# Performance work log

Hardware: AMD Instinct MI355X
Metric: run time of the kernel (lower is better)

Reference implementation:

```python
import jax, jax.numpy as jnp
import numpy as np

N_EMBD = 1024
N_HEAD = 16
HEAD_DIM = N_EMBD // N_HEAD


def setup_inputs() -> dict:
    key = jax.random.key(0)
    kx, kq, kk, kv, ko = jax.random.split(key, 5)
    B, S = 2, 2048
    return {
        "x": jax.random.normal(kx, (B, S, N_EMBD), dtype=jnp.float32),
        "W_q": jax.random.normal(kq, (N_EMBD, N_EMBD), dtype=jnp.float32),
        "W_k": jax.random.normal(kk, (N_EMBD, N_EMBD), dtype=jnp.float32),
        "W_v": jax.random.normal(kv, (N_EMBD, N_EMBD), dtype=jnp.float32),
        "W_o": jax.random.normal(ko, (N_EMBD, N_EMBD), dtype=jnp.float32),
    }


def reference(x, W_q, W_k, W_v, W_o):
    B, S, E = x.shape
    H, D = N_HEAD, HEAD_DIM
    scale = 1.0 / np.sqrt(D).astype(np.float32)
    # QKV projections, split into heads: (B, H, S, D)
    q = (x @ W_q).reshape(B, S, H, D).transpose(0, 2, 1, 3)
    k = (x @ W_k).reshape(B, S, H, D).transpose(0, 2, 1, 3)
    v = (x @ W_v).reshape(B, S, H, D).transpose(0, 2, 1, 3)
    # scaled scores with causal mask
    scores = jnp.einsum("bhqd,bhkd->bhqk", q, k) * scale
    causal = jnp.tril(jnp.ones((S, S), dtype=bool))
    scores = jnp.where(causal, scores, -jnp.inf)
    attn = jax.nn.softmax(scores, axis=-1)
    out = jnp.einsum("bhqk,bhkd->bhqd", attn, v)
    out = out.transpose(0, 2, 1, 3).reshape(B, S, E)
    return out @ W_o
```

## Files before the change

### kernel.cpp

```cpp
#include <hip/hip_runtime.h>
#include <stdint.h>

#define E 1024
#define S 2048
#define NH 16
#define HD 64

typedef _Float16 f16;
typedef _Float16 f16x4 __attribute__((ext_vector_type(4)));
typedef _Float16 f16x8 __attribute__((ext_vector_type(8)));
typedef __fp16 hv4 __attribute__((ext_vector_type(4)));
typedef float f32x4 __attribute__((ext_vector_type(4)));

__device__ __forceinline__ void async16(const void* g, void* l) {
  __builtin_amdgcn_global_load_lds(
      (const __attribute__((address_space(1))) unsigned int*)g,
      (__attribute__((address_space(3))) unsigned int*)l, 16, 0, 0);
}


__global__ __launch_bounds__(256) void cvt_x(const float* __restrict__ x,
                                             f16* __restrict__ xh,
                                             f16* __restrict__ xl) {
  int i = (blockIdx.x * 256 + threadIdx.x) * 4;
  float4 a = *(const float4*)(x + i);
  f16 h0 = (f16)a.x, h1 = (f16)a.y, h2 = (f16)a.z, h3 = (f16)a.w;
  f16x4 hv = {h0, h1, h2, h3};
  f16x4 lv = {(f16)(a.x - (float)h0), (f16)(a.y - (float)h1),
              (f16)(a.z - (float)h2), (f16)(a.w - (float)h3)};
  *(f16x4*)(xh + i) = hv;
  *(f16x4*)(xl + i) = lv;
}

__global__ __launch_bounds__(256) void cvt_w(const float* __restrict__ Wq,
                                             const float* __restrict__ Wk,
                                             const float* __restrict__ Wv,
                                             const float* __restrict__ Wo,
                                             f16* __restrict__ Wh,
                                             f16* __restrict__ Wl) {
  __shared__ float tile[32][33];
  const int z = blockIdx.z;
  const float* W = z == 0 ? Wq : z == 1 ? Wk : z == 2 ? Wv : Wo;
  const int tx = threadIdx.x, ty = threadIdx.y;
  const int x0 = blockIdx.x * 32, y0 = blockIdx.y * 32;
#pragma unroll
  for (int i = 0; i < 4; i++)
    tile[ty + i * 8][tx] = W[(size_t)(y0 + ty + i * 8) * E + x0 + tx];
  __syncthreads();
  f16* outh = Wh + (size_t)z * E * E;
  f16* outl = Wl + (size_t)z * E * E;
#pragma unroll
  for (int i = 0; i < 4; i++) {
    float v = tile[tx][ty + i * 8];
    size_t o = (size_t)(x0 + ty + i * 8) * E + (y0 + tx);
    f16 hi = (f16)v;
    outh[o] = hi;
    if (z < 2) outl[o] = (f16)(v - (float)hi);
  }
}


template <bool SPLIT2>
__device__ __forceinline__ void gemm_mainloop(
    const f16* __restrict__ Ah, const f16* __restrict__ Al,
    const f16* __restrict__ Bh, const f16* __restrict__ Bl, int m0, int n0,
    int K, f16* Ahs, f16* Als, f16* Bhs, f16* Bls, f32x4 acc[4][4]) {
  const int tid = threadIdx.x, lane = tid & 63, wid = tid >> 6;
  const int quad = lane >> 4, c16 = lane & 15;
  const int rA = tid >> 2;
  const int cA = (tid & 3) ^ ((rA >> 1) & 3);
  const size_t gA0 = (size_t)(m0 + rA) * K + cA * 8;
  const size_t gA1 = (size_t)(m0 + 64 + rA) * K + cA * 8;
  const size_t gB0 = (size_t)(n0 + rA) * K + cA * 8;
  const size_t gB1 = (size_t)(n0 + 64 + rA) * K + cA * 8;
  const int l0 = tid * 8, l1 = (256 + tid) * 8;
  int a_off[4], b_off[4];
#pragma unroll
  for (int i = 0; i < 4; i++) {
    int ra = (wid >> 1) * 64 + i * 16 + c16;
    a_off[i] = ra * 32 + ((quad ^ ((ra >> 1) & 3)) << 3);
    int rb = (wid & 1) * 64 + i * 16 + c16;
    b_off[i] = rb * 32 + ((quad ^ ((rb >> 1) & 3)) << 3);
  }
  for (int k0 = 0; k0 < K; k0 += 32) {
    __syncthreads();
    async16(Ah + gA0 + k0, Ahs + l0);
    async16(Ah + gA1 + k0, Ahs + l1);
    async16(Bh + gB0 + k0, Bhs + l0);
    async16(Bh + gB1 + k0, Bhs + l1);
    if constexpr (SPLIT2) {
      async16(Al + gA0 + k0, Als + l0);
      async16(Al + gA1 + k0, Als + l1);
      async16(Bl + gB0 + k0, Bls + l0);
      async16(Bl + gB1 + k0, Bls + l1);
    }
    __syncthreads();
    f16x8 ah[4], bh[4];
#pragma unroll
    for (int i = 0; i < 4; i++) {
      ah[i] = *(const f16x8*)(Ahs + a_off[i]);
      bh[i] = *(const f16x8*)(Bhs + b_off[i]);
    }
    if constexpr (SPLIT2) {
      f16x8 al[4], bl[4];
#pragma unroll
      for (int i = 0; i < 4; i++) {
        al[i] = *(const f16x8*)(Als + a_off[i]);
        bl[i] = *(const f16x8*)(Bls + b_off[i]);
      }
#pragma unroll
      for (int i = 0; i < 4; i++)
#pragma unroll
        for (int j = 0; j < 4; j++) {
          acc[i][j] = __builtin_amdgcn_mfma_f32_16x16x32_f16(ah[i], bh[j], acc[i][j], 0, 0, 0);
          acc[i][j] = __builtin_amdgcn_mfma_f32_16x16x32_f16(ah[i], bl[j], acc[i][j], 0, 0, 0);
          acc[i][j] = __builtin_amdgcn_mfma_f32_16x16x32_f16(al[i], bh[j], acc[i][j], 0, 0, 0);
        }
    } else {
#pragma unroll
      for (int i = 0; i < 4; i++)
#pragma unroll
        for (int j = 0; j < 4; j++)
          acc[i][j] = __builtin_amdgcn_mfma_f32_16x16x32_f16(ah[i], bh[j], acc[i][j], 0, 0, 0);
    }
  }
}

__global__ __launch_bounds__(256) void qkv_gemm(
    const f16* __restrict__ xh, const f16* __restrict__ xl,
    const f16* __restrict__ Wh, const f16* __restrict__ Wl,
    f16* __restrict__ Qh, f16* __restrict__ Ql, f16* __restrict__ Kh,
    f16* __restrict__ Kl, f16* __restrict__ Vt) {
  __shared__ __align__(16) char smem_raw[36864];
  f16* Ahs = (f16*)smem_raw;
  f16* Als = Ahs + 4096;
  f16* Bhs = Ahs + 8192;
  f16* Bls = Ahs + 12288;
  const int z = blockIdx.z;
  const int m0 = blockIdx.y * 128, n0 = blockIdx.x * 128;
  const f16* Bth = Wh + (size_t)z * E * E;
  const f16* Btl = Wl + (size_t)z * E * E;
  f32x4 acc[4][4];
  const f32x4 zero4 = {0.f, 0.f, 0.f, 0.f};
#pragma unroll
  for (int i = 0; i < 4; i++)
#pragma unroll
    for (int j = 0; j < 4; j++) acc[i][j] = zero4;
  if (z < 2)
    gemm_mainloop<true>(xh, xl, Bth, Btl, m0, n0, E, Ahs, Als, Bhs, Bls, acc);
  else
    gemm_mainloop<false>(xh, nullptr, Bth, nullptr, m0, n0, E, Ahs, Als, Bhs, Bls, acc);
  const int tid = threadIdx.x, lane = tid & 63, wid = tid >> 6;
  const int quad = lane >> 4, c16 = lane & 15;
  __syncthreads();
  f16* vbuf = (f16*)smem_raw + (size_t)wid * 4608;
  if (z == 2) {
#pragma unroll
    for (int i = 0; i < 4; i++)
#pragma unroll
      for (int j = 0; j < 4; j++)
#pragma unroll
        for (int r = 0; r < 4; r++) {
          int sl = i * 16 + quad * 4 + r;
          int dl = j * 16 + c16;
          vbuf[dl * 72 + sl] = (f16)acc[i][j][r];
        }
#pragma unroll
    for (int i2 = 0; i2 < 8; i2++) {
      int dl = i2 * 8 + (lane >> 3);
      int ck = lane & 7;
      f16x8 v8 = *(const f16x8*)(vbuf + dl * 72 + ck * 8);
      int dg = n0 + (wid & 1) * 64 + dl;
      int sg = m0 + (wid >> 1) * 64 + ck * 8;
      int b = sg >> 11, s = sg & (S - 1);
      int h = dg >> 6, d = dg & 63;
      *(f16x8*)(Vt + (((size_t)(b * NH + h) * HD + d) << 11) + s) = v8;
    }
  } else {
    const int t0 = m0 + (wid >> 1) * 64;
    const int h = (n0 + (wid & 1) * 64) >> 6;
    const float sc = 0.42466090014400953f;
    f16* dsth = (z == 0) ? Qh : Kh;
    f16* dstl = (z == 0) ? Ql : Kl;
#pragma unroll
    for (int pass = 0; pass < 2; pass++) {
#pragma unroll
      for (int i = 0; i < 4; i++)
#pragma unroll
        for (int j = 0; j < 4; j++)
#pragma unroll
          for (int r = 0; r < 4; r++) {
            float v = acc[i][j][r] * sc;
            f16 hi = (f16)v;
            f16 outv = (pass == 0) ? hi : (f16)(v - (float)hi);
            vbuf[(i * 16 + quad * 4 + r) * 72 + j * 16 + c16] = outv;
          }
      f16* dst = (pass == 0) ? dsth : dstl;
#pragma unroll
      for (int it = 0; it < 8; it++) {
        int row = it * 8 + (lane >> 3);
        int ck = lane & 7;
        f16x8 v8 = *(const f16x8*)(vbuf + row * 72 + ck * 8);
        int tok = t0 + row;
        int b = tok >> 11, s = tok & (S - 1);
        *(f16x8*)(dst + (((size_t)(b * NH + h) * S + s) << 6) + ck * 8) = v8;
      }
    }
  }
}

__global__ __launch_bounds__(256, 3) void flash(
    const f16* __restrict__ Qh, const f16* __restrict__ Ql,
    const f16* __restrict__ Kh, const f16* __restrict__ Kl,
    const f16* __restrict__ Vt, f16* __restrict__ Ao) {
  __shared__ __align__(16) f16 Khs[2][4096], Kls[2][4096], Vs[2][4096];
  const int tid = threadIdx.x, lane = tid & 63, wid = tid >> 6;
  const int quad = lane >> 4, c16 = lane & 15;
  const int flat = blockIdx.y * 32 + blockIdx.x;
  const int xcd = flat & 7, slot = flat >> 3;
  const int bh = xcd * 4 + (slot >> 5);
  const int qtile = 31 - (slot & 31);
  const int q0 = qtile * 64;
  const size_t bhoff = (size_t)bh * S * HD;
  const int qbase = wid * 16;
  f16x8 qf_h[2], qf_l[2];
#pragma unroll
  for (int ks = 0; ks < 2; ks++) {
    int q = q0 + qbase + c16;
    size_t off = bhoff + (size_t)q * HD + ks * 32 + quad * 8;
    qf_h[ks] = *(const f16x8*)(Qh + off);
    qf_l[ks] = *(const f16x8*)(Ql + off);
  }
  const int niter = qtile + 1;
  const int s0 = tid, s1 = 256 + tid;
  const int r0 = s0 >> 3, cc0 = ((s0 & 7) ^ (r0 & 7)) * 8;
  const int r1 = s1 >> 3, cc1 = ((s1 & 7) ^ (r1 & 7)) * 8;
  auto stage = [&](int it, int b) {
    const size_t kb = bhoff + (size_t)(it * 64) * HD;
    async16(Kh + kb + r0 * HD + cc0, &Khs[b][s0 * 8]);
    async16(Kh + kb + r1 * HD + cc1, &Khs[b][s1 * 8]);
    async16(Kl + kb + r0 * HD + cc0, &Kls[b][s0 * 8]);
    async16(Kl + kb + r1 * HD + cc1, &Kls[b][s1 * 8]);
    const size_t vb = bhoff + (size_t)(it * 64);
    async16(Vt + vb + (size_t)r0 * S + cc0, &Vs[b][s0 * 8]);
    async16(Vt + vb + (size_t)r1 * S + cc1, &Vs[b][s1 * 8]);
  };
  stage(0, 0);
  float mrow = -3.0e38f, lsum = 0.f;
  f32x4 oacc[4];
  const f32x4 zero4 = {0.f, 0.f, 0.f, 0.f};
#pragma unroll
  for (int dt = 0; dt < 4; dt++) oacc[dt] = zero4;
  const int qrow = q0 + qbase + c16;
  for (int it = 0; it < niter; ++it) {
    const int cur = it & 1;
    __syncthreads();
    if (it + 1 < niter) stage(it + 1, cur ^ 1);
    const int k0 = it * 64;
    f32x4 st[4];
#pragma unroll
    for (int kt = 0; kt < 4; kt++) st[kt] = zero4;
#pragma unroll
    for (int kt = 0; kt < 4; kt++) {
      int rowk = (kt * 16 + c16) * 64;
      int sx = c16 & 7;
      f16x8 kh0 = *(const f16x8*)&Khs[cur][rowk + ((quad ^ sx) << 3)];
      f16x8 kh1 = *(const f16x8*)&Khs[cur][rowk + (((4 + quad) ^ sx) << 3)];
      f16x8 kl0 = *(const f16x8*)&Kls[cur][rowk + ((quad ^ sx) << 3)];
      f16x8 kl1 = *(const f16x8*)&Kls[cur][rowk + (((4 + quad) ^ sx) << 3)];
      st[kt] = __builtin_amdgcn_mfma_f32_16x16x32_f16(kh0, qf_h[0], st[kt], 0, 0, 0);
      st[kt] = __builtin_amdgcn_mfma_f32_16x16x32_f16(kh1, qf_h[1], st[kt], 0, 0, 0);
      st[kt] = __builtin_amdgcn_mfma_f32_16x16x32_f16(kh0, qf_l[0], st[kt], 0, 0, 0);
      st[kt] = __builtin_amdgcn_mfma_f32_16x16x32_f16(kh1, qf_l[1], st[kt], 0, 0, 0);
      st[kt] = __builtin_amdgcn_mfma_f32_16x16x32_f16(kl0, qf_h[0], st[kt], 0, 0, 0);
      st[kt] = __builtin_amdgcn_mfma_f32_16x16x32_f16(kl1, qf_h[1], st[kt], 0, 0, 0);
    }
    if (it == niter - 1) {
#pragma unroll
      for (int kt = 0; kt < 4; kt++) {
        int kb = k0 + kt * 16 + quad * 4;
#pragma unroll
        for (int r = 0; r < 4; r++)
          if (kb + r > qrow) st[kt][r] = -3.0e38f;
      }
    }
    float mx = -3.0e38f;
#pragma unroll
    for (int kt = 0; kt < 4; kt++) {
      float a = fmaxf(fmaxf(st[kt][0], st[kt][1]), fmaxf(st[kt][2], st[kt][3]));
      mx = fmaxf(mx, a);
    }
    mx = fmaxf(mx, __shfl_xor(mx, 16, 64));
    mx = fmaxf(mx, __shfl_xor(mx, 32, 64));
    float mn = fmaxf(mrow, mx);
    float alpha = __builtin_amdgcn_exp2f(mrow - mn);
    mrow = mn;
    float ls = lsum * alpha;
    hv4 pb[4];
#pragma unroll
    for (int kt = 0; kt < 4; kt++) {
      float p0 = __builtin_amdgcn_exp2f(st[kt][0] - mn);
      float p1 = __builtin_amdgcn_exp2f(st[kt][1] - mn);
      float p2 = __builtin_amdgcn_exp2f(st[kt][2] - mn);
      float p3 = __builtin_amdgcn_exp2f(st[kt][3] - mn);
      ls += (p0 + p1) + (p2 + p3);
      hv4 pv = {(__fp16)p0, (__fp16)p1, (__fp16)p2, (__fp16)p3};
      pb[kt] = pv;
    }
    lsum = ls;
#pragma unroll
    for (int dt = 0; dt < 4; dt++) {
      oacc[dt][0] *= alpha;
      oacc[dt][1] *= alpha;
      oacc[dt][2] *= alpha;
      oacc[dt][3] *= alpha;
    }
#pragma unroll
    for (int kt = 0; kt < 4; kt++) {
#pragma unroll
      for (int dt = 0; dt < 4; dt++) {
        int rowd = dt * 16 + c16;
        int cidx = (kt * 2 + (quad >> 1)) ^ (rowd & 7);
        hv4 vf = *(const hv4*)&Vs[cur][rowd * 64 + (cidx << 3) + (quad & 1) * 4];
        oacc[dt] = __builtin_amdgcn_mfma_f32_16x16x16f16(vf, pb[kt], oacc[dt], 0, 0, 0);
      }
    }
  }
  const int bb = bh >> 4, hh = bh & 15;
  float l = lsum;
  l += __shfl_xor(l, 16, 64);
  l += __shfl_xor(l, 32, 64);
  float iv = 1.0f / l;
  const int q = q0 + qbase + c16;
#pragma unroll
  for (int dt = 0; dt < 4; dt++) {
    f16x4 ov = {(f16)(oacc[dt][0] * iv), (f16)(oacc[dt][1] * iv),
                (f16)(oacc[dt][2] * iv), (f16)(oacc[dt][3] * iv)};
    *(f16x4*)(Ao + ((size_t)(bb * S + q)) * E + hh * 64 + dt * 16 + quad * 4) = ov;
  }
}

__global__ __launch_bounds__(256) void out_gemm(const f16* __restrict__ Ao,
                                                const f16* __restrict__ Wo,
                                                float* __restrict__ Cout) {
  __shared__ __align__(16) f16 Ahs[4096], Bhs[4096];
  const int m0 = blockIdx.y * 128, n0 = blockIdx.x * 128;
  f32x4 acc[4][4];
  const f32x4 zero4 = {0.f, 0.f, 0.f, 0.f};
#pragma unroll
  for (int i = 0; i < 4; i++)
#pragma unroll
    for (int j = 0; j < 4; j++) acc[i][j] = zero4;
  gemm_mainloop<false>(Ao, nullptr, Wo, nullptr, m0, n0, E, Ahs, nullptr, Bhs, nullptr, acc);
  const int lane = threadIdx.x & 63, wid = threadIdx.x >> 6;
  const int quad = lane >> 4, c16 = lane & 15;
#pragma unroll
  for (int i = 0; i < 4; i++)
#pragma unroll
    for (int j = 0; j < 4; j++)
#pragma unroll
      for (int r = 0; r < 4; r++) {
        int row = m0 + (wid >> 1) * 64 + i * 16 + quad * 4 + r;
        int col = n0 + (wid & 1) * 64 + j * 16 + c16;
        Cout[(size_t)row * E + col] = acc[i][j][r];
      }
}

extern "C" void kernel_launch(void* const* d_in, const int* in_sizes, int n_in,
                              void* d_out, int out_size, void* d_ws,
                              size_t ws_size, hipStream_t stream) {
  const float* x = (const float*)d_in[0];
  const float* Wq = (const float*)d_in[1];
  const float* Wk = (const float*)d_in[2];
  const float* Wv = (const float*)d_in[3];
  const float* Wo = (const float*)d_in[4];
  char* ws = (char*)d_ws;
  const size_t MB = (size_t)1 << 20;
  f16* xh = (f16*)(ws + 0 * MB);
  f16* xl = (f16*)(ws + 8 * MB);
  f16* Wh = (f16*)(ws + 16 * MB);
  f16* Wl = (f16*)(ws + 24 * MB);
  f16* Qh = (f16*)(ws + 28 * MB);
  f16* Ql = (f16*)(ws + 36 * MB);
  f16* Kh = (f16*)(ws + 44 * MB);
  f16* Kl = (f16*)(ws + 52 * MB);
  f16* Vt = (f16*)(ws + 60 * MB);
  f16* Ao = (f16*)(ws + 68 * MB);
  cvt_x<<<4096, 256, 0, stream>>>(x, xh, xl);
  cvt_w<<<dim3(32, 32, 4), dim3(32, 8), 0, stream>>>(Wq, Wk, Wv, Wo, Wh, Wl);
  qkv_gemm<<<dim3(8, 32, 3), 256, 0, stream>>>(xh, xl, Wh, Wl, Qh, Ql, Kh, Kl, Vt);
  flash<<<dim3(32, 32), 256, 0, stream>>>(Qh, Ql, Kh, Kl, Vt, Ao);
  out_gemm<<<dim3(8, 32), 256, 0, stream>>>(Ao, Wh + (size_t)3 * E * E, (float*)d_out);
}
```

Measured before the change: 276.3 us.

## Merge conversion kernels, write Q/K directly, retile output GEMM to 64x128

Fuses the x and weight fp32-to-fp16 split conversions into one launch to save a kernel launch. The Q/K epilogue of the QKV GEMM drops its shared-memory staging and writes scalar fp16 values straight to global memory. The output projection gets its own single-buffered 64x128 tile loop with swizzled LDS and twice as many blocks. The direct Q/K writes are scattered 2-byte stores instead of 16-byte vectors, and the new out_gemm loop has no double buffering, so both may lose efficiency.

```diff
diff --git a/kernel.cpp b/kernel.cpp
--- a/kernel.cpp
+++ b/kernel.cpp
@@ -18,30 +18,31 @@
       (__attribute__((address_space(3))) unsigned int*)l, 16, 0, 0);
 }
 
-
-__global__ __launch_bounds__(256) void cvt_x(const float* __restrict__ x,
-                                             f16* __restrict__ xh,
-                                             f16* __restrict__ xl) {
-  int i = (blockIdx.x * 256 + threadIdx.x) * 4;
-  float4 a = *(const float4*)(x + i);
-  f16 h0 = (f16)a.x, h1 = (f16)a.y, h2 = (f16)a.z, h3 = (f16)a.w;
-  f16x4 hv = {h0, h1, h2, h3};
-  f16x4 lv = {(f16)(a.x - (float)h0), (f16)(a.y - (float)h1),
-              (f16)(a.z - (float)h2), (f16)(a.w - (float)h3)};
-  *(f16x4*)(xh + i) = hv;
-  *(f16x4*)(xl + i) = lv;
-}
-
-__global__ __launch_bounds__(256) void cvt_w(const float* __restrict__ Wq,
-                                             const float* __restrict__ Wk,
-                                             const float* __restrict__ Wv,
-                                             const float* __restrict__ Wo,
-                                             f16* __restrict__ Wh,
-                                             f16* __restrict__ Wl) {
+__global__ __launch_bounds__(256) void cvt_all(
+    const float* __restrict__ x, const float* __restrict__ Wq,
+    const float* __restrict__ Wk, const float* __restrict__ Wv,
+    const float* __restrict__ Wo, f16* __restrict__ xh, f16* __restrict__ xl,
+    f16* __restrict__ Wh, f16* __restrict__ Wl) {
+  const int z = blockIdx.z;
+  const int tid = threadIdx.x;
+  if (z == 4) {
+    int base = ((blockIdx.y * 32 + blockIdx.x) * 256 + tid) * 16;
+#pragma unroll
+    for (int u = 0; u < 4; u++) {
+      int i = base + u * 4;
+      float4 a = *(const float4*)(x + i);
+      f16 h0 = (f16)a.x, h1 = (f16)a.y, h2 = (f16)a.z, h3 = (f16)a.w;
+      f16x4 hv = {h0, h1, h2, h3};
+      f16x4 lv = {(f16)(a.x - (float)h0), (f16)(a.y - (float)h1),
+                  (f16)(a.z - (float)h2), (f16)(a.w - (float)h3)};
+      *(f16x4*)(xh + i) = hv;
+      *(f16x4*)(xl + i) = lv;
+    }
+    return;
+  }
   __shared__ float tile[32][33];
-  const int z = blockIdx.z;
   const float* W = z == 0 ? Wq : z == 1 ? Wk : z == 2 ? Wv : Wo;
-  const int tx = threadIdx.x, ty = threadIdx.y;
+  const int tx = tid & 31, ty = tid >> 5;
   const int x0 = blockIdx.x * 32, y0 = blockIdx.y * 32;
 #pragma unroll
   for (int i = 0; i < 4; i++)
@@ -152,9 +153,9 @@
     gemm_mainloop<false>(xh, nullptr, Bth, nullptr, m0, n0, E, Ahs, Als, Bhs, Bls, acc);
   const int tid = threadIdx.x, lane = tid & 63, wid = tid >> 6;
   const int quad = lane >> 4, c16 = lane & 15;
-  __syncthreads();
-  f16* vbuf = (f16*)smem_raw + (size_t)wid * 4608;
   if (z == 2) {
+    __syncthreads();
+    f16* vbuf = (f16*)smem_raw + (size_t)wid * 4608;
 #pragma unroll
     for (int i = 0; i < 4; i++)
 #pragma unroll
@@ -177,35 +178,24 @@
       *(f16x8*)(Vt + (((size_t)(b * NH + h) * HD + d) << 11) + s) = v8;
     }
   } else {
-    const int t0 = m0 + (wid >> 1) * 64;
-    const int h = (n0 + (wid & 1) * 64) >> 6;
     const float sc = 0.42466090014400953f;
-    f16* dsth = (z == 0) ? Qh : Kh;
-    f16* dstl = (z == 0) ? Ql : Kl;
-#pragma unroll
-    for (int pass = 0; pass < 2; pass++) {
-#pragma unroll
-      for (int i = 0; i < 4; i++)
-#pragma unroll
-        for (int j = 0; j < 4; j++)
-#pragma unroll
-          for (int r = 0; r < 4; r++) {
-            float v = acc[i][j][r] * sc;
-            f16 hi = (f16)v;
-            f16 outv = (pass == 0) ? hi : (f16)(v - (float)hi);
-            vbuf[(i * 16 + quad * 4 + r) * 72 + j * 16 + c16] = outv;
-          }
-      f16* dst = (pass == 0) ? dsth : dstl;
-#pragma unroll
-      for (int it = 0; it < 8; it++) {
-        int row = it * 8 + (lane >> 3);
-        int ck = lane & 7;
-        f16x8 v8 = *(const f16x8*)(vbuf + row * 72 + ck * 8);
-        int tok = t0 + row;
-        int b = tok >> 11, s = tok & (S - 1);
-        *(f16x8*)(dst + (((size_t)(b * NH + h) * S + s) << 6) + ck * 8) = v8;
-      }
-    }
+#pragma unroll
+    for (int i = 0; i < 4; i++)
+#pragma unroll
+      for (int j = 0; j < 4; j++)
+#pragma unroll
+        for (int r = 0; r < 4; r++) {
+          int row = m0 + (wid >> 1) * 64 + i * 16 + quad * 4 + r;
+          int col = n0 + (wid & 1) * 64 + j * 16 + c16;
+          int b = row >> 11, s = row & (S - 1);
+          int h = col >> 6, d = col & 63;
+          float v = acc[i][j][r] * sc;
+          size_t idx = (((size_t)(b * NH + h) * S + s) << 6) + d;
+          f16 hi = (f16)v;
+          f16 lo = (f16)(v - (float)hi);
+          if (z == 0) { Qh[idx] = hi; Ql[idx] = lo; }
+          else        { Kh[idx] = hi; Kl[idx] = lo; }
+        }
   }
 }
 
@@ -343,25 +333,58 @@
 __global__ __launch_bounds__(256) void out_gemm(const f16* __restrict__ Ao,
                                                 const f16* __restrict__ Wo,
                                                 float* __restrict__ Cout) {
-  __shared__ __align__(16) f16 Ahs[4096], Bhs[4096];
-  const int m0 = blockIdx.y * 128, n0 = blockIdx.x * 128;
-  f32x4 acc[4][4];
+  __shared__ __align__(16) f16 Ahs[2048], Bhs[4096];
+  const int tid = threadIdx.x, lane = tid & 63, wid = tid >> 6;
+  const int quad = lane >> 4, c16 = lane & 15;
+  const int m0 = blockIdx.y * 64, n0 = blockIdx.x * 128;
+  f32x4 acc[4][2];
   const f32x4 zero4 = {0.f, 0.f, 0.f, 0.f};
 #pragma unroll
   for (int i = 0; i < 4; i++)
 #pragma unroll
-    for (int j = 0; j < 4; j++) acc[i][j] = zero4;
-  gemm_mainloop<false>(Ao, nullptr, Wo, nullptr, m0, n0, E, Ahs, nullptr, Bhs, nullptr, acc);
-  const int lane = threadIdx.x & 63, wid = threadIdx.x >> 6;
-  const int quad = lane >> 4, c16 = lane & 15;
+    for (int j = 0; j < 2; j++) acc[i][j] = zero4;
+  const int rA = tid >> 2;
+  const int cA = (tid & 3) ^ ((rA >> 1) & 3);
+  const size_t gA0 = (size_t)(m0 + rA) * E + cA * 8;
+  const size_t gB0 = (size_t)(n0 + rA) * E + cA * 8;
+  const size_t gB1 = (size_t)(n0 + 64 + rA) * E + cA * 8;
+  const int l0 = tid * 8, l1 = (256 + tid) * 8;
+  int a_off[4], b_off[2];
+#pragma unroll
+  for (int i = 0; i < 4; i++) {
+    int ra = i * 16 + c16;
+    a_off[i] = ra * 32 + ((quad ^ ((ra >> 1) & 3)) << 3);
+  }
+#pragma unroll
+  for (int j = 0; j < 2; j++) {
+    int rb = wid * 32 + j * 16 + c16;
+    b_off[j] = rb * 32 + ((quad ^ ((rb >> 1) & 3)) << 3);
+  }
+  for (int k0 = 0; k0 < E; k0 += 32) {
+    __syncthreads();
+    async16(Ao + gA0 + k0, Ahs + l0);
+    async16(Wo + gB0 + k0, Bhs + l0);
+    async16(Wo + gB1 + k0, Bhs + l1);
+    __syncthreads();
+    f16x8 ah[4], bh[2];
+#pragma unroll
+    for (int i = 0; i < 4; i++) ah[i] = *(const f16x8*)(Ahs + a_off[i]);
+#pragma unroll
+    for (int j = 0; j < 2; j++) bh[j] = *(const f16x8*)(Bhs + b_off[j]);
+#pragma unroll
+    for (int i = 0; i < 4; i++)
+#pragma unroll
+      for (int j = 0; j < 2; j++)
+        acc[i][j] = __builtin_amdgcn_mfma_f32_16x16x32_f16(ah[i], bh[j], acc[i][j], 0, 0, 0);
+  }
 #pragma unroll
   for (int i = 0; i < 4; i++)
 #pragma unroll
-    for (int j = 0; j < 4; j++)
+    for (int j = 0; j < 2; j++)
 #pragma unroll
       for (int r = 0; r < 4; r++) {
-        int row = m0 + (wid >> 1) * 64 + i * 16 + quad * 4 + r;
-        int col = n0 + (wid & 1) * 64 + j * 16 + c16;
+        int row = m0 + i * 16 + quad * 4 + r;
+        int col = n0 + wid * 32 + j * 16 + c16;
         Cout[(size_t)row * E + col] = acc[i][j][r];
       }
 }
@@ -386,9 +409,8 @@
   f16* Kl = (f16*)(ws + 52 * MB);
   f16* Vt = (f16*)(ws + 60 * MB);
   f16* Ao = (f16*)(ws + 68 * MB);
-  cvt_x<<<4096, 256, 0, stream>>>(x, xh, xl);
-  cvt_w<<<dim3(32, 32, 4), dim3(32, 8), 0, stream>>>(Wq, Wk, Wv, Wo, Wh, Wl);
+  cvt_all<<<dim3(32, 32, 5), 256, 0, stream>>>(x, Wq, Wk, Wv, Wo, xh, xl, Wh, Wl);
   qkv_gemm<<<dim3(8, 32, 3), 256, 0, stream>>>(xh, xl, Wh, Wl, Qh, Ql, Kh, Kl, Vt);
   flash<<<dim3(32, 32), 256, 0, stream>>>(Qh, Ql, Kh, Kl, Vt, Ao);
-  out_gemm<<<dim3(8, 32), 256, 0, stream>>>(Ao, Wh + (size_t)3 * E * E, (float*)d_out);
-}
+  out_gemm<<<dim3(8, 64), 256, 0, stream>>>(Ao, Wh + (size_t)3 * E * E, (float*)d_out);
+}
```

New measurement: 241.4 us. 1.14x faster.
